# Kernel optimization log

Hardware: AMD Instinct MI355X
Metric: run time of the kernel (lower is better)

The kernel has to match this reference:

```python
import jax, jax.numpy as jnp
import numpy as np
from jax import lax

BATCH, L, DM, N = 16, 4096, 256, 16


def setup_inputs() -> dict:
    key = jax.random.key(0)
    ks = jax.random.split(key, 8)
    s = lambda k, shape: jax.random.normal(k, shape, dtype=jnp.float32) * 0.05
    A_log = jnp.tile(jnp.log(jnp.arange(1, N + 1, dtype=jnp.float32))[None, :], (DM, 1))
    return {
        "x": jax.random.normal(ks[0], (BATCH, L, DM), dtype=jnp.float32),
        "A_log": A_log,                      # [D, N]
        "D_skip": jnp.ones((DM,), jnp.float32),
        "W_B": s(ks[1], (N, DM)),
        "W_C": s(ks[2], (N, DM)),
        "W_delta": s(ks[3], (DM, DM)),
        "b_delta": jnp.zeros((DM,), jnp.float32),
        "W_in": s(ks[4], (2 * DM, DM)),
        "b_in": jnp.zeros((2 * DM,), jnp.float32),
        "W_out": s(ks[5], (DM, DM)),
        "b_out": jnp.zeros((DM,), jnp.float32),
        "conv_w": s(ks[6], (DM, 1, 3)),      # depthwise conv1d weight (groups=D)
        "conv_b": jnp.zeros((DM,), jnp.float32),
    }


def reference(x, A_log, D_skip, W_B, W_C, W_delta, b_delta, W_in, b_in, W_out, b_out, conv_w, conv_b):
    A = -jnp.exp(A_log)                                   # [D, N]
    xz = x @ W_in.T + b_in                                # [B, L, 2D]
    x_in, z = jnp.split(xz, 2, axis=-1)
    # depthwise conv over time (padding=1, kernel=3, groups=D)
    xc = lax.conv_general_dilated(
        x_in.transpose(0, 2, 1), conv_w, window_strides=(1,),
        padding=[(1, 1)], dimension_numbers=("NCH", "OIH", "NCH"),
        feature_group_count=DM)
    xc = (xc + conv_b[None, :, None]).transpose(0, 2, 1)  # [B, L, D]
    xc = jax.nn.silu(xc)
    delta = jax.nn.softplus(xc @ W_delta.T + b_delta)     # [B, L, D]
    B_sel = xc @ W_B.T                                    # [B, L, N]
    C_sel = xc @ W_C.T                                    # [B, L, N]

    def step(h, inp):
        dt, b_t, c_t, u_t = inp                           # [B,D],[B,N],[B,N],[B,D]
        A_bar = jnp.exp(dt[..., None] * A)                # [B, D, N]
        h = A_bar * h + (dt * u_t)[..., None] * b_t[:, None, :]
        y_t = jnp.sum(h * c_t[:, None, :], axis=-1)       # [B, D]
        return h, y_t

    h0 = jnp.zeros((x.shape[0], DM, N), dtype=x.dtype)
    xs = (delta.transpose(1, 0, 2), B_sel.transpose(1, 0, 2),
          C_sel.transpose(1, 0, 2), xc.transpose(1, 0, 2))
    _, ys = lax.scan(step, h0, xs)                        # ys: [L, B, D]
    y = ys.transpose(1, 0, 2) + xc * D_skip               # skip applied in use_conv branch
    y = y * jax.nn.silu(z)
    return y @ W_out.T + b_out
```

## Files before the change

### kernel.cpp

```cpp
#include <hip/hip_runtime.h>
#include <hip/hip_bf16.h>
#include <math.h>

#define BATCH 16
#define LSEQ 4096
#define DMODEL 256
#define NST 16
#define LC 64
#define NCHB (LSEQ / LC)
#define MROWS (BATCH * LSEQ)
#define LOG2E 1.44269504088896340736f
#define LN2 0.6931471805599453f

typedef float f32x4 __attribute__((ext_vector_type(4)));
typedef float f32x2 __attribute__((ext_vector_type(2)));
typedef short bf16x8 __attribute__((ext_vector_type(8)));

__device__ __forceinline__ float silu_fast(float v) {
  return v * __builtin_amdgcn_rcpf(1.f + __builtin_amdgcn_exp2f(-v * LOG2E));
}
__device__ __forceinline__ float softplus_fast(float v) {
  float l = LN2 * __builtin_amdgcn_logf(1.f + __builtin_amdgcn_exp2f(v * LOG2E));
  return v > 16.f ? v : l;
}
__device__ __forceinline__ uint bf16rne(float f) {
  uint u = __float_as_uint(f);
  return (u + 0x7fffu + ((u >> 16) & 1u)) >> 16;
}
__device__ __forceinline__ float bf2f(ushort u) {
  return __uint_as_float((uint)u << 16);
}
__device__ __forceinline__ ushort f2h(float v) {
  _Float16 h = (_Float16)v;
  return __builtin_bit_cast(ushort, h);
}
__device__ __forceinline__ float h2f(ushort u) {
  return (float)__builtin_bit_cast(_Float16, u);
}
__device__ __forceinline__ uint pk2(float x, float y) {
  return bf16rne(x) | (bf16rne(y) << 16);
}
__device__ __forceinline__ uint4 pk8(float4 a, float4 b) {
  uint4 r;
  r.x = pk2(a.x, a.y);
  r.y = pk2(a.z, a.w);
  r.z = pk2(b.x, b.y);
  r.w = pk2(b.z, b.w);
  return r;
}
__device__ __forceinline__ void ub8(uint4 v, float* o) {
  o[0] = bf2f((ushort)(v.x & 0xffff));
  o[1] = bf2f((ushort)(v.x >> 16));
  o[2] = bf2f((ushort)(v.y & 0xffff));
  o[3] = bf2f((ushort)(v.y >> 16));
  o[4] = bf2f((ushort)(v.z & 0xffff));
  o[5] = bf2f((ushort)(v.z >> 16));
  o[6] = bf2f((ushort)(v.w & 0xffff));
  o[7] = bf2f((ushort)(v.w >> 16));
}

__device__ __forceinline__ void pow8pk(float e1, int s, f32x2* p) {
  float e2 = e1 * e1;
  p[0] = f32x2{e1, e2};
  f32x2 e2v = {e2, e2};
  p[1] = p[0] * e2v;
  f32x2 e4v = {p[1].y, p[1].y};
  p[2] = p[0] * e4v;
  p[3] = p[1] * e4v;
  float sel = s ? p[3].y : 1.0f;
  f32x2 selv = {sel, sel};
  p[0] *= selv;
  p[1] *= selv;
  p[2] *= selv;
  p[3] *= selv;
}

__device__ __forceinline__ void glds16(const ushort* g, char* l) {
  __builtin_amdgcn_global_load_lds(
      (const __attribute__((address_space(1))) void*)g,
      (__attribute__((address_space(3))) void*)l, 16, 0, 0);
}

__device__ __forceinline__ void stageB512(const ushort* gbase, char* dst,
                                          int k0, int lane, int wid) {
#pragma unroll
  for (int c = 0; c < 2; ++c) {
    int r = (wid * 2 + c) * 16 + (lane >> 2);
    int sA = (r + (r >> 2)) & 3;
    int cA = (lane & 3) ^ sA;
    glds16(gbase + (size_t)r * 256 + cA * 8 + k0, dst + (wid * 2 + c) * 1024);
  }
}

__global__ __launch_bounds__(256) void cvt_weights(
    const float* __restrict__ Win, const float* __restrict__ Wd,
    const float* __restrict__ Wo, const float* __restrict__ WB,
    const float* __restrict__ WC, ushort* __restrict__ dst) {
  size_t i = ((size_t)blockIdx.x * 256 + threadIdx.x) * 8;
  if (i >= 270336) return;
  const float* s;
  size_t o;
  if (i < 131072)      { s = Win; o = i; }
  else if (i < 196608) { s = Wd;  o = i - 131072; }
  else if (i < 262144) { s = Wo;  o = i - 196608; }
  else if (i < 266240) { s = WB;  o = i - 262144; }
  else                 { s = WC;  o = i - 266240; }
  float4 a = *(const float4*)(s + o);
  float4 b = *(const float4*)(s + o + 4);
  *(uint4*)(dst + i) = pk8(a, b);
}

__global__ __launch_bounds__(256, 4) void gemm_in(
    const float* __restrict__ A, const ushort* __restrict__ Bbf,
    const float* __restrict__ bias, ushort* __restrict__ out0,
    ushort* __restrict__ out1) {
  constexpr int KD = 256;
  __shared__ char smem[40960];
  const int tid = threadIdx.x;
  const int lane = tid & 63, wid = tid >> 6;
  const int M0 = blockIdx.y * 64;
  const int N0 = blockIdx.x * 256;

  const int rA = tid >> 2, cA = tid & 3;
  const int sA = (rA + (rA >> 2)) & 3;
  const int ldsAoff = rA * 64 + ((cA ^ sA) * 16);
  const float* gA32 = A + (size_t)(M0 + rA) * KD + cA * 8;
  const ushort* gB = Bbf + (size_t)(N0 + rA) * KD + ((cA ^ sA) * 8);

  f32x4 acc[4][4];
#pragma unroll
  for (int i = 0; i < 4; ++i)
#pragma unroll
    for (int j = 0; j < 4; ++j) acc[i][j] = {0.f, 0.f, 0.f, 0.f};

  {
#pragma unroll
    for (int i = 0; i < 4; ++i)
      glds16(gB + (size_t)i * 64 * KD, smem + 4096 + i * 4096 + wid * 1024);
    float4 a0 = *(const float4*)(gA32);
    float4 a1 = *(const float4*)(gA32 + 4);
    *(uint4*)(smem + ldsAoff) = pk8(a0, a1);
  }
  __syncthreads();

  for (int step = 0; step < 8; ++step) {
    const int cur = step & 1;
    char* bufc = smem + cur * 20480;
    char* bufn = smem + (cur ^ 1) * 20480;
    float4 na0, na1;
    if (step < 7) {
      const int k0 = (step + 1) * 32;
#pragma unroll
      for (int i = 0; i < 4; ++i)
        glds16(gB + (size_t)i * 64 * KD + k0,
               bufn + 4096 + i * 4096 + wid * 1024);
      na0 = *(const float4*)(gA32 + k0);
      na1 = *(const float4*)(gA32 + k0 + 4);
    }
    bf16x8 af[4], bfr[4];
#pragma unroll
    for (int i = 0; i < 4; ++i) {
      int r = i * 16 + (lane & 15);
      int slot = (lane >> 4) ^ ((r + (r >> 2)) & 3);
      af[i] = *(const bf16x8*)(bufc + r * 64 + slot * 16);
    }
#pragma unroll
    for (int j = 0; j < 4; ++j) {
      int r = wid * 64 + j * 16 + (lane & 15);
      int slot = (lane >> 4) ^ ((r + (r >> 2)) & 3);
      bfr[j] = *(const bf16x8*)(bufc + 4096 + r * 64 + slot * 16);
    }
#pragma unroll
    for (int i = 0; i < 4; ++i)
#pragma unroll
      for (int j = 0; j < 4; ++j)
        acc[i][j] = __builtin_amdgcn_mfma_f32_16x16x32_bf16(af[i], bfr[j],
                                                            acc[i][j], 0, 0, 0);
    if (step < 7) *(uint4*)(bufn + ldsAoff) = pk8(na0, na1);
    __syncthreads();
  }

  const int rbase = (lane >> 4) * 4;
  const int cn = lane & 15;
#pragma unroll
  for (int i = 0; i < 4; ++i) {
#pragma unroll
    for (int j = 0; j < 4; ++j) {
      int col = N0 + wid * 64 + j * 16 + cn;
      float bs = bias[col];
#pragma unroll
      for (int r = 0; r < 4; ++r) {
        int row = M0 + i * 16 + rbase + r;
        float v = acc[i][j][r] + bs;
        if (col < DMODEL)
          out0[(size_t)row * DMODEL + col] = (ushort)bf16rne(v);
        else
          out1[(size_t)row * DMODEL + (col - DMODEL)] =
              (ushort)bf16rne(silu_fast(v));
      }
    }
  }
}

__global__ __launch_bounds__(512, 4) void fused_mid(
    const ushort* __restrict__ xin, const ushort* __restrict__ wdl,
    const ushort* __restrict__ wbc, const float* __restrict__ b_delta,
    const float* __restrict__ A_log, const float* __restrict__ conv_w,
    const float* __restrict__ conv_b, ushort* __restrict__ xc_g,
    ushort* __restrict__ dl_g, ushort* __restrict__ bc_g,
    float* __restrict__ hout, float* __restrict__ cumA) {
  __shared__ char smem[73728];
  const int tid = threadIdx.x, lane = tid & 63, wid = tid >> 6;
  const int b = blockIdx.x / NCHB, c = blockIdx.x % NCHB;
  const int l0 = c * LC;
  const size_t row0 = (size_t)b * LSEQ + l0;

  {
#pragma unroll
    for (int cc = 0; cc < 2; ++cc) {
      int row = (wid * 2 + cc) * 2 + (lane >> 5);
      int cB = (lane & 31) ^ (row & 7);
      glds16(wbc + (size_t)row * 256 + cB * 8,
             smem + 49152 + (wid * 2 + cc) * 1024);
    }
  }
  stageB512(wdl, smem + 32768, 0, lane, wid);

  {
    const int dq = tid & 31;
    const int d0 = dq * 8;
    float w0[8], w1[8], w2[8], cb[8];
#pragma unroll
    for (int k = 0; k < 8; ++k) {
      w0[k] = conv_w[(d0 + k) * 3 + 0];
      w1[k] = conv_w[(d0 + k) * 3 + 1];
      w2[k] = conv_w[(d0 + k) * 3 + 2];
      cb[k] = conv_b[d0 + k];
    }
#pragma unroll
    for (int it = 0; it < 4; ++it) {
      const int lr = it * 16 + (tid >> 5);
      const int l = l0 + lr;
      const size_t bp = (row0 + lr) * DMODEL + d0;
      uint4 zf4 = {0u, 0u, 0u, 0u};
      uint4 um = (l > 0) ? *(const uint4*)(xin + bp - DMODEL) : zf4;
      uint4 uc4 = *(const uint4*)(xin + bp);
      uint4 up = (l < LSEQ - 1) ? *(const uint4*)(xin + bp + DMODEL) : zf4;
      float mv[8], cv[8], pv[8], ov[8];
      ub8(um, mv);
      ub8(uc4, cv);
      ub8(up, pv);
#pragma unroll
      for (int k = 0; k < 8; ++k) {
        float o = fmaf(w0[k], mv[k], fmaf(w1[k], cv[k], fmaf(w2[k], pv[k], cb[k])));
        ov[k] = silu_fast(o);
      }
      uint4 r4;
      r4.x = pk2(ov[0], ov[1]);
      r4.y = pk2(ov[2], ov[3]);
      r4.z = pk2(ov[4], ov[5]);
      r4.w = pk2(ov[6], ov[7]);
      *(uint4*)(xc_g + bp) = r4;
      *(uint4*)(smem + lr * 512 + ((dq ^ (lr & 7)) * 16)) = r4;
    }
  }
  __syncthreads();

  f32x4 acc[4][2];
#pragma unroll
  for (int i = 0; i < 4; ++i)
#pragma unroll
    for (int j = 0; j < 2; ++j) acc[i][j] = {0.f, 0.f, 0.f, 0.f};
  f32x4 accbc = {0.f, 0.f, 0.f, 0.f};

  for (int step = 0; step < 8; ++step) {
    bf16x8 af[4], bfr[2];
#pragma unroll
    for (int i = 0; i < 4; ++i) {
      int r = i * 16 + (lane & 15);
      int sc = step * 4 + (lane >> 4);
      af[i] = *(const bf16x8*)(smem + r * 512 + ((sc ^ (r & 7)) * 16));
    }
#pragma unroll
    for (int j = 0; j < 2; ++j) {
      int r = wid * 32 + j * 16 + (lane & 15);
      int slot = (lane >> 4) ^ ((r + (r >> 2)) & 3);
      bfr[j] = *(const bf16x8*)(smem + 32768 + r * 64 + slot * 16);
    }
#pragma unroll
    for (int i = 0; i < 4; ++i)
#pragma unroll
      for (int j = 0; j < 2; ++j)
        acc[i][j] = __builtin_amdgcn_mfma_f32_16x16x32_bf16(af[i], bfr[j],
                                                            acc[i][j], 0, 0, 0);
    __syncthreads();
    if (step < 7) stageB512(wdl, smem + 32768, (step + 1) * 32, lane, wid);
    {
      int sc = step * 4 + (lane >> 4);
      int ra = (wid >> 1) * 16 + (lane & 15);
      bf16x8 a2 = *(const bf16x8*)(smem + ra * 512 + ((sc ^ (ra & 7)) * 16));
      int br = (wid & 1) * 16 + (lane & 15);
      bf16x8 b2 =
          *(const bf16x8*)(smem + 49152 + br * 512 + ((sc ^ (br & 7)) * 16));
      accbc = __builtin_amdgcn_mfma_f32_16x16x32_bf16(a2, b2, accbc, 0, 0, 0);
    }
    __syncthreads();
  }

  const int rbase = (lane >> 4) * 4;
  const int cn = lane & 15;
#pragma unroll
  for (int i = 0; i < 4; ++i)
#pragma unroll
    for (int j = 0; j < 2; ++j) {
      int col = wid * 32 + j * 16 + cn;
      float bs = b_delta[col];
#pragma unroll
      for (int r = 0; r < 4; ++r) {
        int row = i * 16 + rbase + r;
        *(ushort*)(smem + 32768 + row * 512 +
                   ((col * 2) ^ (((row >> 2) & 3) << 5))) =
            f2h(softplus_fast(acc[i][j][r] + bs));
      }
    }
  {
#pragma unroll
    for (int r = 0; r < 4; ++r) {
      int row = (wid >> 1) * 16 + rbase + r;
      int col = (wid & 1) * 16 + cn;
      ushort bv = (ushort)bf16rne(accbc[r]);
      ((float*)(smem + 65536))[row * 32 + col] = bf2f(bv);
      bc_g[(row0 + row) * 32 + col] = bv;
    }
  }
  __syncthreads();

#pragma unroll
  for (int it = 0; it < 4; ++it) {
    int idx = it * 512 + tid;
    int row = idx >> 5, ch = idx & 31;
    *(uint4*)(dl_g + (row0 + row) * DMODEL + ch * 8) =
        *(const uint4*)(smem + 32768 + row * 512 +
                        ((ch ^ (((row >> 2) & 3) << 1)) * 16));
  }

  const int d = tid >> 1;
  const int s = tid & 1;
  float Aa2h[8];
  {
    float4 v0 = *(const float4*)(A_log + d * NST + 8 * s);
    float4 v1 = *(const float4*)(A_log + d * NST + 8 * s + 4);
    Aa2h[0] = -LOG2E * __expf(v0.x);
    Aa2h[1] = -LOG2E * __expf(v0.y);
    Aa2h[2] = -LOG2E * __expf(v0.z);
    Aa2h[3] = -LOG2E * __expf(v0.w);
    Aa2h[4] = -LOG2E * __expf(v1.x);
    Aa2h[5] = -LOG2E * __expf(v1.y);
    Aa2h[6] = -LOG2E * __expf(v1.z);
    Aa2h[7] = -LOG2E * __expf(v1.w);
  }
  const float Aa2_0 = -LOG2E * __expf(A_log[d * NST]);
  bool pm = true;
#pragma unroll
  for (int k = 0; k < 8; ++k)
    pm = pm && (fabsf(Aa2h[k] - (float)(8 * s + k + 1) * Aa2_0) <=
                1e-3f * fabsf(Aa2h[k]));

  float sdt = 0.f;
  const int uoff0 = (d & 7) * 2;
  const int uchunk = d >> 3;
  if (pm) {
    f32x2 h2[4];
#pragma unroll
    for (int q = 0; q < 4; ++q) h2[q] = f32x2{0.f, 0.f};
#pragma unroll 4
    for (int l = 0; l < LC; ++l) {
      float dt = h2f(*(const ushort*)(smem + 32768 + l * 512 +
                                      ((d * 2) ^ (((l >> 2) & 3) << 5))));
      float u = bf2f(*(const ushort*)(smem + l * 512 +
                                      ((uchunk ^ (l & 7)) * 16) + uoff0));
      sdt += dt;
      float dtu = dt * u;
      f32x2 dtu2 = {dtu, dtu};
      const float* Bp = (const float*)(smem + 65536) + l * 32 + 8 * s;
      f32x4 B0 = *(const f32x4*)(Bp);
      f32x4 B1 = *(const f32x4*)(Bp + 4);
      f32x2 p[4];
      pow8pk(__builtin_amdgcn_exp2f(dt * Aa2_0), s, p);
      h2[0] = p[0] * h2[0] + dtu2 * B0.xy;
      h2[1] = p[1] * h2[1] + dtu2 * B0.zw;
      h2[2] = p[2] * h2[2] + dtu2 * B1.xy;
      h2[3] = p[3] * h2[3] + dtu2 * B1.zw;
    }
    f32x2 cum[4];
    pow8pk(__builtin_amdgcn_exp2f(sdt * Aa2_0), s, cum);
    const size_t ob =
        (((size_t)(b * NCHB + c)) * DMODEL + d) * NST + 8 * s;
    float4 hv0 = {h2[0].x, h2[0].y, h2[1].x, h2[1].y};
    float4 hv1 = {h2[2].x, h2[2].y, h2[3].x, h2[3].y};
    *(float4*)(hout + ob) = hv0;
    *(float4*)(hout + ob + 4) = hv1;
    float4 cv0 = {cum[0].x, cum[0].y, cum[1].x, cum[1].y};
    float4 cv1 = {cum[2].x, cum[2].y, cum[3].x, cum[3].y};
    *(float4*)(cumA + ob) = cv0;
    *(float4*)(cumA + ob + 4) = cv1;
  } else {
    float h[8];
#pragma unroll
    for (int k = 0; k < 8; ++k) h[k] = 0.f;
#pragma unroll 4
    for (int l = 0; l < LC; ++l) {
      float dt = h2f(*(const ushort*)(smem + 32768 + l * 512 +
                                      ((d * 2) ^ (((l >> 2) & 3) << 5))));
      float u = bf2f(*(const ushort*)(smem + l * 512 +
                                      ((uchunk ^ (l & 7)) * 16) + uoff0));
      sdt += dt;
      float dtu = dt * u;
      const float* Bp = (const float*)(smem + 65536) + l * 32 + 8 * s;
      f32x4 B0 = *(const f32x4*)(Bp);
      f32x4 B1 = *(const f32x4*)(Bp + 4);
      float Bv[8] = {B0.x, B0.y, B0.z, B0.w, B1.x, B1.y, B1.z, B1.w};
#pragma unroll
      for (int k = 0; k < 8; ++k) {
        float ab = __builtin_amdgcn_exp2f(dt * Aa2h[k]);
        h[k] = fmaf(ab, h[k], dtu * Bv[k]);
      }
    }
    const size_t ob =
        (((size_t)(b * NCHB + c)) * DMODEL + d) * NST + 8 * s;
#pragma unroll
    for (int q = 0; q < 2; ++q) {
      float4 hv = {h[q * 4 + 0], h[q * 4 + 1], h[q * 4 + 2], h[q * 4 + 3]};
      *(float4*)(hout + ob + q * 4) = hv;
      float4 cvv = {__builtin_amdgcn_exp2f(sdt * Aa2h[q * 4 + 0]),
                    __builtin_amdgcn_exp2f(sdt * Aa2h[q * 4 + 1]),
                    __builtin_amdgcn_exp2f(sdt * Aa2h[q * 4 + 2]),
                    __builtin_amdgcn_exp2f(sdt * Aa2h[q * 4 + 3])};
      *(float4*)(cumA + ob + q * 4) = cvv;
    }
  }
}

__global__ __launch_bounds__(256) void scan_combine(
    float* __restrict__ hstate, const float* __restrict__ cumA) {
  const int t = blockIdx.x * 256 + threadIdx.x;
  const int n = t & (NST - 1);
  const int dd = (t / NST) & (DMODEL - 1);
  const int b = t / (NST * DMODEL);
  float h = 0.f;
  for (int c = 0; c < NCHB; ++c) {
    size_t idx = (((size_t)(b * NCHB + c)) * DMODEL + dd) * NST + n;
    float ho = hstate[idx];
    float ca = cumA[idx];
    hstate[idx] = h;
    h = fmaf(ca, h, ho);
  }
}

__global__ __launch_bounds__(512, 4) void fused_out(
    const ushort* __restrict__ dl, const ushort* __restrict__ xcb,
    const ushort* __restrict__ szy, const ushort* __restrict__ bcb,
    const float* __restrict__ A_log, const float* __restrict__ hin,
    const float* __restrict__ Dskip, const ushort* __restrict__ wout,
    const float* __restrict__ b_out, float* __restrict__ out) {
  __shared__ char smem[73728];
  const int tid = threadIdx.x, lane = tid & 63, wid = tid >> 6;
  const int b = blockIdx.x / NCHB, c = blockIdx.x % NCHB;
  const int l0 = c * LC;
  const size_t row0 = (size_t)b * LSEQ + l0;

  {
    int r = tid >> 3, q = tid & 7;
    uint2 v = *(const uint2*)(bcb + (row0 + r) * 32 + q * 4);
    float* dp = (float*)(smem + 65536) + r * 32 + q * 4;
    dp[0] = bf2f((ushort)(v.x & 0xffff));
    dp[1] = bf2f((ushort)(v.x >> 16));
    dp[2] = bf2f((ushort)(v.y & 0xffff));
    dp[3] = bf2f((ushort)(v.y >> 16));
  }
  stageB512(wout, smem + 32768, 0, lane, wid);

  const int d = tid >> 1;
  const int s = tid & 1;
  float Aa2h[8];
  {
    float4 v0 = *(const float4*)(A_log + d * NST + 8 * s);
    float4 v1 = *(const float4*)(A_log + d * NST + 8 * s + 4);
    Aa2h[0] = -LOG2E * __expf(v0.x);
    Aa2h[1] = -LOG2E * __expf(v0.y);
    Aa2h[2] = -LOG2E * __expf(v0.z);
    Aa2h[3] = -LOG2E * __expf(v0.w);
    Aa2h[4] = -LOG2E * __expf(v1.x);
    Aa2h[5] = -LOG2E * __expf(v1.y);
    Aa2h[6] = -LOG2E * __expf(v1.z);
    Aa2h[7] = -LOG2E * __expf(v1.w);
  }
  const float Aa2_0 = -LOG2E * __expf(A_log[d * NST]);
  bool pm = true;
#pragma unroll
  for (int k = 0; k < 8; ++k)
    pm = pm && (fabsf(Aa2h[k] - (float)(8 * s + k + 1) * Aa2_0) <=
                1e-3f * fabsf(Aa2h[k]));
  f32x2 h2[4];
  const size_t hb =
      (((size_t)(b * NCHB + c)) * DMODEL + d) * NST + 8 * s;
  {
    float4 v0 = *(const float4*)(hin + hb);
    float4 v1 = *(const float4*)(hin + hb + 4);
    h2[0] = f32x2{v0.x, v0.y};
    h2[1] = f32x2{v0.z, v0.w};
    h2[2] = f32x2{v1.x, v1.y};
    h2[3] = f32x2{v1.z, v1.w};
  }
  const float dsk = Dskip[d];
  __syncthreads();

  const size_t base = row0 * DMODEL + d;
  const int ywoff = (d & 7) * 2;
  const int ywchunk = d >> 3;
  ushort dtr[4], ur[4], zr[4];
#pragma unroll
  for (int j = 0; j < 4; ++j) {
    dtr[j] = dl[base + (size_t)j * DMODEL];
    ur[j] = xcb[base + (size_t)j * DMODEL];
    if (s == 0) zr[j] = szy[base + (size_t)j * DMODEL];
  }
  for (int lb = 0; lb < LC / 4; ++lb) {
    ushort dtn[4], un[4], zn[4];
    if (lb < LC / 4 - 1) {
      size_t nb = base + (size_t)(lb * 4 + 4) * DMODEL;
#pragma unroll
      for (int j = 0; j < 4; ++j) {
        dtn[j] = dl[nb + (size_t)j * DMODEL];
        un[j] = xcb[nb + (size_t)j * DMODEL];
        if (s == 0) zn[j] = szy[nb + (size_t)j * DMODEL];
      }
    }
#pragma unroll
    for (int j = 0; j < 4; ++j) {
      int l = lb * 4 + j;
      float dt = h2f(dtr[j]);
      float u = bf2f(ur[j]);
      float dtu = dt * u;
      f32x2 dtu2 = {dtu, dtu};
      const float* Bp = (const float*)(smem + 65536) + l * 32 + 8 * s;
      f32x4 B0 = *(const f32x4*)(Bp);
      f32x4 B1 = *(const f32x4*)(Bp + 4);
      f32x4 C0 = *(const f32x4*)(Bp + 16);
      f32x4 C1 = *(const f32x4*)(Bp + 20);
      float y;
      if (pm) {
        f32x2 p[4];
        pow8pk(__builtin_amdgcn_exp2f(dt * Aa2_0), s, p);
        f32x2 y2 = {0.f, 0.f};
        h2[0] = p[0] * h2[0] + dtu2 * B0.xy;
        y2 = y2 + h2[0] * C0.xy;
        h2[1] = p[1] * h2[1] + dtu2 * B0.zw;
        y2 = y2 + h2[1] * C0.zw;
        h2[2] = p[2] * h2[2] + dtu2 * B1.xy;
        y2 = y2 + h2[2] * C1.xy;
        h2[3] = p[3] * h2[3] + dtu2 * B1.zw;
        y2 = y2 + h2[3] * C1.zw;
        y = y2.x + y2.y;
      } else {
        float Bv[8] = {B0.x, B0.y, B0.z, B0.w, B1.x, B1.y, B1.z, B1.w};
        float Cv[8] = {C0.x, C0.y, C0.z, C0.w, C1.x, C1.y, C1.z, C1.w};
        float hs[8] = {h2[0].x, h2[0].y, h2[1].x, h2[1].y,
                       h2[2].x, h2[2].y, h2[3].x, h2[3].y};
        y = 0.f;
#pragma unroll
        for (int k = 0; k < 8; ++k) {
          float ab = __builtin_amdgcn_exp2f(dt * Aa2h[k]);
          hs[k] = fmaf(ab, hs[k], dtu * Bv[k]);
          y = fmaf(hs[k], Cv[k], y);
        }
        h2[0] = f32x2{hs[0], hs[1]};
        h2[1] = f32x2{hs[2], hs[3]};
        h2[2] = f32x2{hs[4], hs[5]};
        h2[3] = f32x2{hs[6], hs[7]};
      }
      y += __shfl_xor(y, 1);
      if (s == 0) {
        float yp = (y + u * dsk) * bf2f(zr[j]);
        *(ushort*)(smem + l * 512 + ((ywchunk ^ (l & 7)) * 16) + ywoff) =
            (ushort)bf16rne(yp);
      }
    }
#pragma unroll
    for (int j = 0; j < 4; ++j) {
      dtr[j] = dtn[j];
      ur[j] = un[j];
      if (s == 0) zr[j] = zn[j];
    }
  }
  __syncthreads();

  f32x4 acc[4][2];
#pragma unroll
  for (int i = 0; i < 4; ++i)
#pragma unroll
    for (int j = 0; j < 2; ++j) acc[i][j] = {0.f, 0.f, 0.f, 0.f};

  for (int step = 0; step < 8; ++step) {
    char* bufc = smem + 32768 + (step & 1) * 16384;
    if (step < 7)
      stageB512(wout, smem + 32768 + ((step + 1) & 1) * 16384,
                (step + 1) * 32, lane, wid);
    bf16x8 af[4], bfr[2];
#pragma unroll
    for (int i = 0; i < 4; ++i) {
      int r = i * 16 + (lane & 15);
      int sc = step * 4 + (lane >> 4);
      af[i] = *(const bf16x8*)(smem + r * 512 + ((sc ^ (r & 7)) * 16));
    }
#pragma unroll
    for (int j = 0; j < 2; ++j) {
      int r = wid * 32 + j * 16 + (lane & 15);
      int slot = (lane >> 4) ^ ((r + (r >> 2)) & 3);
      bfr[j] = *(const bf16x8*)(bufc + r * 64 + slot * 16);
    }
#pragma unroll
    for (int i = 0; i < 4; ++i)
#pragma unroll
      for (int j = 0; j < 2; ++j)
        acc[i][j] = __builtin_amdgcn_mfma_f32_16x16x32_bf16(af[i], bfr[j],
                                                            acc[i][j], 0, 0, 0);
    __syncthreads();
  }

  const int rbase = (lane >> 4) * 4;
  const int cn = lane & 15;
#pragma unroll
  for (int i = 0; i < 4; ++i)
#pragma unroll
    for (int j = 0; j < 2; ++j) {
      int col = wid * 32 + j * 16 + cn;
      float bs = b_out[col];
#pragma unroll
      for (int r = 0; r < 4; ++r) {
        int row = i * 16 + rbase + r;
        out[(row0 + row) * DMODEL + col] = acc[i][j][r] + bs;
      }
    }
}

extern "C" void kernel_launch(void* const* d_in, const int* in_sizes, int n_in,
                              void* d_out, int out_size, void* d_ws,
                              size_t ws_size, hipStream_t stream) {
  const float* x       = (const float*)d_in[0];
  const float* A_log   = (const float*)d_in[1];
  const float* D_skip  = (const float*)d_in[2];
  const float* W_B     = (const float*)d_in[3];
  const float* W_C     = (const float*)d_in[4];
  const float* W_delta = (const float*)d_in[5];
  const float* b_delta = (const float*)d_in[6];
  const float* W_in    = (const float*)d_in[7];
  const float* b_in    = (const float*)d_in[8];
  const float* W_out   = (const float*)d_in[9];
  const float* b_out   = (const float*)d_in[10];
  const float* conv_w  = (const float*)d_in[11];
  const float* conv_b  = (const float*)d_in[12];

  const size_t MD = (size_t)MROWS * DMODEL;
  const size_t HP = (size_t)BATCH * NCHB * DMODEL * NST;
  ushort* xinb = (ushort*)d_ws;
  ushort* dl   = xinb + MD;
  ushort* szy  = dl + MD;
  ushort* xcb  = szy + MD;
  ushort* bcb  = xcb + MD;
  float* hst   = (float*)(bcb + (size_t)MROWS * 32);
  float* cumA  = hst + HP;
  ushort* wbf  = (ushort*)(cumA + HP);

  cvt_weights<<<dim3(132), 256, 0, stream>>>(W_in, W_delta, W_out, W_B, W_C, wbf);
  gemm_in<<<dim3(2, MROWS / 64), 256, 0, stream>>>(x, wbf, b_in, xinb, szy);
  fused_mid<<<dim3(BATCH * NCHB), 512, 0, stream>>>(
      xinb, wbf + 131072, wbf + 262144, b_delta, A_log, conv_w, conv_b,
      xcb, dl, bcb, hst, cumA);
  scan_combine<<<dim3(BATCH * DMODEL * NST / 256), 256, 0, stream>>>(hst, cumA);
  fused_out<<<dim3(BATCH * NCHB), 512, 0, stream>>>(
      dl, xcb, szy, bcb, A_log, hst, D_skip, wbf + 196608, b_out,
      (float*)d_out);
}
```

Baseline: 197.0 us.

## Split fused_out scan across four threads per channel with 1024-thread blocks

The fused_out kernel now uses 1024 threads per block, giving each channel four threads that each own 4 of the 16 state entries instead of two threads owning 8. Per-thread serial recurrence work and register use drop, and the output GEMM is redistributed so that 16 waves each compute one 16-column tile. The cost is an extra cross-lane shuffle reduction per timestep, more threads idle during the y write, and launch bounds of (1024, 8), which constrain registers and occupancy.

```diff
diff --git a/kernel.cpp b/kernel.cpp
--- a/kernel.cpp
+++ b/kernel.cpp
@@ -75,6 +75,19 @@
   p[3] *= selv;
 }
 
+__device__ __forceinline__ void pow4pk(float e1, int s2, f32x2* p) {
+  float e2 = e1 * e1;
+  p[0] = f32x2{e1, e2};
+  f32x2 e2v = {e2, e2};
+  p[1] = p[0] * e2v;
+  float e4 = p[1].y;
+  float e8 = e4 * e4;
+  float sel = (s2 == 0) ? 1.0f : (s2 == 1) ? e4 : (s2 == 2) ? e8 : e8 * e4;
+  f32x2 selv = {sel, sel};
+  p[0] *= selv;
+  p[1] *= selv;
+}
+
 __device__ __forceinline__ void glds16(const ushort* g, char* l) {
   __builtin_amdgcn_global_load_lds(
       (const __attribute__((address_space(1))) void*)g,
@@ -90,6 +103,13 @@
     int cA = (lane & 3) ^ sA;
     glds16(gbase + (size_t)r * 256 + cA * 8 + k0, dst + (wid * 2 + c) * 1024);
   }
+}
+__device__ __forceinline__ void stageB1024(const ushort* gbase, char* dst,
+                                           int k0, int lane, int wid) {
+  int r = wid * 16 + (lane >> 2);
+  int sA = (r + (r >> 2)) & 3;
+  int cA = (lane & 3) ^ sA;
+  glds16(gbase + (size_t)r * 256 + cA * 8 + k0, dst + wid * 1024);
 }
 
 __global__ __launch_bounds__(256) void cvt_weights(
@@ -457,7 +477,7 @@
   }
 }
 
-__global__ __launch_bounds__(512, 4) void fused_out(
+__global__ __launch_bounds__(1024, 8) void fused_out(
     const ushort* __restrict__ dl, const ushort* __restrict__ xcb,
     const ushort* __restrict__ szy, const ushort* __restrict__ bcb,
     const float* __restrict__ A_log, const float* __restrict__ hin,
@@ -470,47 +490,38 @@
   const size_t row0 = (size_t)b * LSEQ + l0;
 
   {
-    int r = tid >> 3, q = tid & 7;
-    uint2 v = *(const uint2*)(bcb + (row0 + r) * 32 + q * 4);
-    float* dp = (float*)(smem + 65536) + r * 32 + q * 4;
-    dp[0] = bf2f((ushort)(v.x & 0xffff));
-    dp[1] = bf2f((ushort)(v.x >> 16));
-    dp[2] = bf2f((ushort)(v.y & 0xffff));
-    dp[3] = bf2f((ushort)(v.y >> 16));
-  }
-  stageB512(wout, smem + 32768, 0, lane, wid);
-
-  const int d = tid >> 1;
-  const int s = tid & 1;
-  float Aa2h[8];
-  {
-    float4 v0 = *(const float4*)(A_log + d * NST + 8 * s);
-    float4 v1 = *(const float4*)(A_log + d * NST + 8 * s + 4);
+    int t2 = tid * 2;
+    int r = t2 >> 5, co = t2 & 31;
+    uint v = *(const uint*)(bcb + (row0 + r) * 32 + co);
+    float* dp = (float*)(smem + 65536) + r * 32 + co;
+    dp[0] = bf2f((ushort)(v & 0xffff));
+    dp[1] = bf2f((ushort)(v >> 16));
+  }
+  stageB1024(wout, smem + 32768, 0, lane, wid);
+
+  const int d = tid >> 2;
+  const int s2 = tid & 3;
+  float Aa2h[4];
+  {
+    float4 v0 = *(const float4*)(A_log + d * NST + 4 * s2);
     Aa2h[0] = -LOG2E * __expf(v0.x);
     Aa2h[1] = -LOG2E * __expf(v0.y);
     Aa2h[2] = -LOG2E * __expf(v0.z);
     Aa2h[3] = -LOG2E * __expf(v0.w);
-    Aa2h[4] = -LOG2E * __expf(v1.x);
-    Aa2h[5] = -LOG2E * __expf(v1.y);
-    Aa2h[6] = -LOG2E * __expf(v1.z);
-    Aa2h[7] = -LOG2E * __expf(v1.w);
   }
   const float Aa2_0 = -LOG2E * __expf(A_log[d * NST]);
   bool pm = true;
 #pragma unroll
-  for (int k = 0; k < 8; ++k)
-    pm = pm && (fabsf(Aa2h[k] - (float)(8 * s + k + 1) * Aa2_0) <=
+  for (int k = 0; k < 4; ++k)
+    pm = pm && (fabsf(Aa2h[k] - (float)(4 * s2 + k + 1) * Aa2_0) <=
                 1e-3f * fabsf(Aa2h[k]));
-  f32x2 h2[4];
+  f32x2 h2[2];
   const size_t hb =
-      (((size_t)(b * NCHB + c)) * DMODEL + d) * NST + 8 * s;
+      (((size_t)(b * NCHB + c)) * DMODEL + d) * NST + 4 * s2;
   {
     float4 v0 = *(const float4*)(hin + hb);
-    float4 v1 = *(const float4*)(hin + hb + 4);
     h2[0] = f32x2{v0.x, v0.y};
     h2[1] = f32x2{v0.z, v0.w};
-    h2[2] = f32x2{v1.x, v1.y};
-    h2[3] = f32x2{v1.z, v1.w};
   }
   const float dsk = Dskip[d];
   __syncthreads();
@@ -523,7 +534,7 @@
   for (int j = 0; j < 4; ++j) {
     dtr[j] = dl[base + (size_t)j * DMODEL];
     ur[j] = xcb[base + (size_t)j * DMODEL];
-    if (s == 0) zr[j] = szy[base + (size_t)j * DMODEL];
+    if (s2 == 0) zr[j] = szy[base + (size_t)j * DMODEL];
   }
   for (int lb = 0; lb < LC / 4; ++lb) {
     ushort dtn[4], un[4], zn[4];
@@ -533,7 +544,7 @@
       for (int j = 0; j < 4; ++j) {
         dtn[j] = dl[nb + (size_t)j * DMODEL];
         un[j] = xcb[nb + (size_t)j * DMODEL];
-        if (s == 0) zn[j] = szy[nb + (size_t)j * DMODEL];
+        if (s2 == 0) zn[j] = szy[nb + (size_t)j * DMODEL];
       }
     }
 #pragma unroll
@@ -543,44 +554,36 @@
       float u = bf2f(ur[j]);
       float dtu = dt * u;
       f32x2 dtu2 = {dtu, dtu};
-      const float* Bp = (const float*)(smem + 65536) + l * 32 + 8 * s;
+      const float* Bp = (const float*)(smem + 65536) + l * 32 + 4 * s2;
       f32x4 B0 = *(const f32x4*)(Bp);
-      f32x4 B1 = *(const f32x4*)(Bp + 4);
       f32x4 C0 = *(const f32x4*)(Bp + 16);
-      f32x4 C1 = *(const f32x4*)(Bp + 20);
       float y;
       if (pm) {
-        f32x2 p[4];
-        pow8pk(__builtin_amdgcn_exp2f(dt * Aa2_0), s, p);
+        f32x2 p[2];
+        pow4pk(__builtin_amdgcn_exp2f(dt * Aa2_0), s2, p);
         f32x2 y2 = {0.f, 0.f};
         h2[0] = p[0] * h2[0] + dtu2 * B0.xy;
         y2 = y2 + h2[0] * C0.xy;
         h2[1] = p[1] * h2[1] + dtu2 * B0.zw;
         y2 = y2 + h2[1] * C0.zw;
-        h2[2] = p[2] * h2[2] + dtu2 * B1.xy;
-        y2 = y2 + h2[2] * C1.xy;
-        h2[3] = p[3] * h2[3] + dtu2 * B1.zw;
-        y2 = y2 + h2[3] * C1.zw;
         y = y2.x + y2.y;
       } else {
-        float Bv[8] = {B0.x, B0.y, B0.z, B0.w, B1.x, B1.y, B1.z, B1.w};
-        float Cv[8] = {C0.x, C0.y, C0.z, C0.w, C1.x, C1.y, C1.z, C1.w};
-        float hs[8] = {h2[0].x, h2[0].y, h2[1].x, h2[1].y,
-                       h2[2].x, h2[2].y, h2[3].x, h2[3].y};
+        float Bv[4] = {B0.x, B0.y, B0.z, B0.w};
+        float Cv[4] = {C0.x, C0.y, C0.z, C0.w};
+        float hs[4] = {h2[0].x, h2[0].y, h2[1].x, h2[1].y};
         y = 0.f;
 #pragma unroll
-        for (int k = 0; k < 8; ++k) {
+        for (int k = 0; k < 4; ++k) {
           float ab = __builtin_amdgcn_exp2f(dt * Aa2h[k]);
           hs[k] = fmaf(ab, hs[k], dtu * Bv[k]);
           y = fmaf(hs[k], Cv[k], y);
         }
         h2[0] = f32x2{hs[0], hs[1]};
         h2[1] = f32x2{hs[2], hs[3]};
-        h2[2] = f32x2{hs[4], hs[5]};
-        h2[3] = f32x2{hs[6], hs[7]};
       }
       y += __shfl_xor(y, 1);
-      if (s == 0) {
+      y += __shfl_xor(y, 2);
+      if (s2 == 0) {
         float yp = (y + u * dsk) * bf2f(zr[j]);
         *(ushort*)(smem + l * 512 + ((ywchunk ^ (l & 7)) * 16) + ywoff) =
             (ushort)bf16rne(yp);
@@ -590,58 +593,51 @@
     for (int j = 0; j < 4; ++j) {
       dtr[j] = dtn[j];
       ur[j] = un[j];
-      if (s == 0) zr[j] = zn[j];
+      if (s2 == 0) zr[j] = zn[j];
     }
   }
   __syncthreads();
 
-  f32x4 acc[4][2];
-#pragma unroll
-  for (int i = 0; i < 4; ++i)
-#pragma unroll
-    for (int j = 0; j < 2; ++j) acc[i][j] = {0.f, 0.f, 0.f, 0.f};
+  f32x4 acc[4];
+#pragma unroll
+  for (int i = 0; i < 4; ++i) acc[i] = {0.f, 0.f, 0.f, 0.f};
 
   for (int step = 0; step < 8; ++step) {
     char* bufc = smem + 32768 + (step & 1) * 16384;
     if (step < 7)
-      stageB512(wout, smem + 32768 + ((step + 1) & 1) * 16384,
-                (step + 1) * 32, lane, wid);
-    bf16x8 af[4], bfr[2];
+      stageB1024(wout, smem + 32768 + ((step + 1) & 1) * 16384,
+                 (step + 1) * 32, lane, wid);
+    bf16x8 af[4], bfr;
 #pragma unroll
     for (int i = 0; i < 4; ++i) {
       int r = i * 16 + (lane & 15);
       int sc = step * 4 + (lane >> 4);
       af[i] = *(const bf16x8*)(smem + r * 512 + ((sc ^ (r & 7)) * 16));
     }
-#pragma unroll
-    for (int j = 0; j < 2; ++j) {
-      int r = wid * 32 + j * 16 + (lane & 15);
+    {
+      int r = wid * 16 + (lane & 15);
       int slot = (lane >> 4) ^ ((r + (r >> 2)) & 3);
-      bfr[j] = *(const bf16x8*)(bufc + r * 64 + slot * 16);
+      bfr = *(const bf16x8*)(bufc + r * 64 + slot * 16);
     }
 #pragma unroll
     for (int i = 0; i < 4; ++i)
-#pragma unroll
-      for (int j = 0; j < 2; ++j)
-        acc[i][j] = __builtin_amdgcn_mfma_f32_16x16x32_bf16(af[i], bfr[j],
-                                                            acc[i][j], 0, 0, 0);
+      acc[i] = __builtin_amdgcn_mfma_f32_16x16x32_bf16(af[i], bfr,
+                                                       acc[i], 0, 0, 0);
     __syncthreads();
   }
 
   const int rbase = (lane >> 4) * 4;
   const int cn = lane & 15;
 #pragma unroll
-  for (int i = 0; i < 4; ++i)
-#pragma unroll
-    for (int j = 0; j < 2; ++j) {
-      int col = wid * 32 + j * 16 + cn;
-      float bs = b_out[col];
-#pragma unroll
-      for (int r = 0; r < 4; ++r) {
-        int row = i * 16 + rbase + r;
-        out[(row0 + row) * DMODEL + col] = acc[i][j][r] + bs;
-      }
-    }
+  for (int i = 0; i < 4; ++i) {
+    int col = wid * 16 + cn;
+    float bs = b_out[col];
+#pragma unroll
+    for (int r = 0; r < 4; ++r) {
+      int row = i * 16 + rbase + r;
+      out[(row0 + row) * DMODEL + col] = acc[i][r] + bs;
+    }
+  }
 }
 
 extern "C" void kernel_launch(void* const* d_in, const int* in_sizes, int n_in,
@@ -678,7 +674,7 @@
       xinb, wbf + 131072, wbf + 262144, b_delta, A_log, conv_w, conv_b,
       xcb, dl, bcb, hst, cumA);
   scan_combine<<<dim3(BATCH * DMODEL * NST / 256), 256, 0, stream>>>(hst, cumA);
-  fused_out<<<dim3(BATCH * NCHB), 512, 0, stream>>>(
+  fused_out<<<dim3(BATCH * NCHB), 1024, 0, stream>>>(
       dl, xcb, szy, bcb, A_log, hst, D_skip, wbf + 196608, b_out,
       (float*)d_out);
 }
```

New measurement: 219.4 us. +11.3%, slower.

## Shrink fused_out LDS: bf16 B/C staging, single-buffer W_out, raise occupancy

Applied to the files above, without the earlier changes.

Keeps B/C selections in LDS as bf16, loaded with a direct global-to-LDS copy and unpacked on read, instead of converting them to fp32 at staging time. Drops the double buffer for W_out tiles in favour of a single buffer with an extra barrier per step. Together these cut shared memory from 72KB to 52KB and raise the launch-bounds occupancy hint from 4 to 6, aiming for more resident blocks to hide latency. The cost is extra unpack ALU work in the scan loop and serialized W_out loads in the GEMM phase, since the next tile is no longer prefetched during the MFMAs.

```diff
diff --git a/kernel.cpp b/kernel.cpp
--- a/kernel.cpp
+++ b/kernel.cpp
@@ -457,27 +457,21 @@
   }
 }
 
-__global__ __launch_bounds__(512, 4) void fused_out(
+__global__ __launch_bounds__(512, 6) void fused_out(
     const ushort* __restrict__ dl, const ushort* __restrict__ xcb,
     const ushort* __restrict__ szy, const ushort* __restrict__ bcb,
     const float* __restrict__ A_log, const float* __restrict__ hin,
     const float* __restrict__ Dskip, const ushort* __restrict__ wout,
     const float* __restrict__ b_out, float* __restrict__ out) {
-  __shared__ char smem[73728];
+  __shared__ char smem[53248];
   const int tid = threadIdx.x, lane = tid & 63, wid = tid >> 6;
   const int b = blockIdx.x / NCHB, c = blockIdx.x % NCHB;
   const int l0 = c * LC;
   const size_t row0 = (size_t)b * LSEQ + l0;
 
-  {
-    int r = tid >> 3, q = tid & 7;
-    uint2 v = *(const uint2*)(bcb + (row0 + r) * 32 + q * 4);
-    float* dp = (float*)(smem + 65536) + r * 32 + q * 4;
-    dp[0] = bf2f((ushort)(v.x & 0xffff));
-    dp[1] = bf2f((ushort)(v.x >> 16));
-    dp[2] = bf2f((ushort)(v.y & 0xffff));
-    dp[3] = bf2f((ushort)(v.y >> 16));
-  }
+  if (wid < 4)
+    glds16(bcb + row0 * 32 + (size_t)(wid * 64 + lane) * 8,
+           smem + 49152 + wid * 1024);
   stageB512(wout, smem + 32768, 0, lane, wid);
 
   const int d = tid >> 1;
@@ -543,36 +537,35 @@
       float u = bf2f(ur[j]);
       float dtu = dt * u;
       f32x2 dtu2 = {dtu, dtu};
-      const float* Bp = (const float*)(smem + 65536) + l * 32 + 8 * s;
-      f32x4 B0 = *(const f32x4*)(Bp);
-      f32x4 B1 = *(const f32x4*)(Bp + 4);
-      f32x4 C0 = *(const f32x4*)(Bp + 16);
-      f32x4 C1 = *(const f32x4*)(Bp + 20);
+      const char* bcrow = smem + 49152 + l * 64;
+      uint4 bu = *(const uint4*)(bcrow + s * 16);
+      uint4 cu = *(const uint4*)(bcrow + 32 + s * 16);
+      float Bf[8], Cf[8];
+      ub8(bu, Bf);
+      ub8(cu, Cf);
       float y;
       if (pm) {
         f32x2 p[4];
         pow8pk(__builtin_amdgcn_exp2f(dt * Aa2_0), s, p);
         f32x2 y2 = {0.f, 0.f};
-        h2[0] = p[0] * h2[0] + dtu2 * B0.xy;
-        y2 = y2 + h2[0] * C0.xy;
-        h2[1] = p[1] * h2[1] + dtu2 * B0.zw;
-        y2 = y2 + h2[1] * C0.zw;
-        h2[2] = p[2] * h2[2] + dtu2 * B1.xy;
-        y2 = y2 + h2[2] * C1.xy;
-        h2[3] = p[3] * h2[3] + dtu2 * B1.zw;
-        y2 = y2 + h2[3] * C1.zw;
+        h2[0] = p[0] * h2[0] + dtu2 * f32x2{Bf[0], Bf[1]};
+        y2 = y2 + h2[0] * f32x2{Cf[0], Cf[1]};
+        h2[1] = p[1] * h2[1] + dtu2 * f32x2{Bf[2], Bf[3]};
+        y2 = y2 + h2[1] * f32x2{Cf[2], Cf[3]};
+        h2[2] = p[2] * h2[2] + dtu2 * f32x2{Bf[4], Bf[5]};
+        y2 = y2 + h2[2] * f32x2{Cf[4], Cf[5]};
+        h2[3] = p[3] * h2[3] + dtu2 * f32x2{Bf[6], Bf[7]};
+        y2 = y2 + h2[3] * f32x2{Cf[6], Cf[7]};
         y = y2.x + y2.y;
       } else {
-        float Bv[8] = {B0.x, B0.y, B0.z, B0.w, B1.x, B1.y, B1.z, B1.w};
-        float Cv[8] = {C0.x, C0.y, C0.z, C0.w, C1.x, C1.y, C1.z, C1.w};
         float hs[8] = {h2[0].x, h2[0].y, h2[1].x, h2[1].y,
                        h2[2].x, h2[2].y, h2[3].x, h2[3].y};
         y = 0.f;
 #pragma unroll
         for (int k = 0; k < 8; ++k) {
           float ab = __builtin_amdgcn_exp2f(dt * Aa2h[k]);
-          hs[k] = fmaf(ab, hs[k], dtu * Bv[k]);
-          y = fmaf(hs[k], Cv[k], y);
+          hs[k] = fmaf(ab, hs[k], dtu * Bf[k]);
+          y = fmaf(hs[k], Cf[k], y);
         }
         h2[0] = f32x2{hs[0], hs[1]};
         h2[1] = f32x2{hs[2], hs[3]};
@@ -602,10 +595,6 @@
     for (int j = 0; j < 2; ++j) acc[i][j] = {0.f, 0.f, 0.f, 0.f};
 
   for (int step = 0; step < 8; ++step) {
-    char* bufc = smem + 32768 + (step & 1) * 16384;
-    if (step < 7)
-      stageB512(wout, smem + 32768 + ((step + 1) & 1) * 16384,
-                (step + 1) * 32, lane, wid);
     bf16x8 af[4], bfr[2];
 #pragma unroll
     for (int i = 0; i < 4; ++i) {
@@ -617,7 +606,7 @@
     for (int j = 0; j < 2; ++j) {
       int r = wid * 32 + j * 16 + (lane & 15);
       int slot = (lane >> 4) ^ ((r + (r >> 2)) & 3);
-      bfr[j] = *(const bf16x8*)(bufc + r * 64 + slot * 16);
+      bfr[j] = *(const bf16x8*)(smem + 32768 + r * 64 + slot * 16);
     }
 #pragma unroll
     for (int i = 0; i < 4; ++i)
@@ -625,6 +614,8 @@
       for (int j = 0; j < 2; ++j)
         acc[i][j] = __builtin_amdgcn_mfma_f32_16x16x32_bf16(af[i], bfr[j],
                                                             acc[i][j], 0, 0, 0);
+    __syncthreads();
+    if (step < 7) stageB512(wout, smem + 32768, (step + 1) * 32, lane, wid);
     __syncthreads();
   }
 
```

After: 214.4 us. 1.09x slower.
